# Optimization experiments

Measured on AMD Instinct MI355X. Metric: run time of the kernel, lower is better.

Reference implementation:

```python
import jax, jax.numpy as jnp
import numpy as np

# Module config (from init_kwargs): Occ3D-nuScenes volume
VOL_MIN = np.array([-40.0, -40.0, -1.0], dtype=np.float32)
VOXEL_SIZE = 0.4
GRID_SHAPE = (200, 200, 16)  # (vol_max - vol_min) / voxel_size
K = 6          # fixed per-gaussian window; covers radii <= 0.6m (bbox span <= 5 voxels)
N_GAUSS = 32768
N_DIMS = 16


def setup_inputs() -> dict:
    key = jax.random.key(0)
    k1, k2, k3, k4, k5 = jax.random.split(key, 5)
    # Means strictly inside the volume with 1m margin so bboxes stay in-grid.
    lo = jnp.array([-39.0, -39.0, 0.0], dtype=jnp.float32)
    hi = jnp.array([39.0, 39.0, 4.4], dtype=jnp.float32)
    means3d = jax.random.uniform(k1, (N_GAUSS, 3), minval=lo, maxval=hi, dtype=jnp.float32)
    # SPD covariances: Q diag(s) Q^T with eigenvalues in [0.01, 0.04]
    A = jax.random.normal(k2, (N_GAUSS, 3, 3), dtype=jnp.float32)
    Q, _ = jnp.linalg.qr(A)
    s = jax.random.uniform(k3, (N_GAUSS, 3), minval=0.01, maxval=0.04, dtype=jnp.float32)
    covs = jnp.einsum('nij,nj,nkj->nik', Q, s, Q)
    opacities = jax.random.uniform(k4, (N_GAUSS,), dtype=jnp.float32)
    features = jax.random.normal(k5, (N_GAUSS, N_DIMS), dtype=jnp.float32)
    return {"means3d": means3d, "covs": covs, "opacities": opacities, "features": features}


def reference(means3d, covs, opacities, features):
    N, D = features.shape
    dim_x, dim_y, dim_z = GRID_SHAPE
    total = dim_x * dim_y * dim_z
    vol_min = jnp.asarray(VOL_MIN)

    inv_covs = jnp.linalg.inv(covs)                                  # [N,3,3]
    radii = 3.0 * jnp.sqrt(jnp.diagonal(covs, axis1=-2, axis2=-1))   # [N,3]

    # Bounding box in voxel indices (trunc toward zero, like the triton .to(int32))
    s = (means3d - radii - vol_min) / VOXEL_SIZE
    e = (means3d + radii - vol_min) / VOXEL_SIZE
    start = jnp.maximum(0, s.astype(jnp.int32))                      # [N,3]
    end = jnp.minimum(jnp.array(GRID_SHAPE, jnp.int32), e.astype(jnp.int32) + 1)

    offs = jnp.arange(K, dtype=jnp.int32)
    ix = start[:, 0:1] + offs   # [N,K]
    iy = start[:, 1:2] + offs
    iz = start[:, 2:3] + offs
    mask = ((ix < end[:, 0:1])[:, :, None, None]
            & (iy < end[:, 1:2])[:, None, :, None]
            & (iz < end[:, 2:3])[:, None, None, :])                  # [N,K,K,K]

    # Voxel-corner minus mean offsets (matches kernel: x*vs + vol_min - m)
    px = ix.astype(means3d.dtype) * VOXEL_SIZE + vol_min[0] - means3d[:, 0:1]  # [N,K]
    py = iy.astype(means3d.dtype) * VOXEL_SIZE + vol_min[1] - means3d[:, 1:2]
    pz = iz.astype(means3d.dtype) * VOXEL_SIZE + vol_min[2] - means3d[:, 2:3]
    d = jnp.stack(jnp.broadcast_arrays(px[:, :, None, None],
                                       py[:, None, :, None],
                                       pz[:, None, None, :]), axis=-1)  # [N,K,K,K,3]

    mahal = jnp.einsum('nxyzi,nij,nxyzj->nxyz', d, inv_covs, d)      # [N,K,K,K]
    density = opacities[:, None, None, None] * jnp.exp(-0.5 * mahal)
    density = jnp.where(mask, density, 0.0)

    flat_idx = (ix[:, :, None, None] * (dim_y * dim_z)
                + iy[:, None, :, None] * dim_z
                + iz[:, None, None, :])                               # [N,K,K,K]
    idx = flat_idx.reshape(-1)

    grid_density = jnp.zeros((total,), density.dtype).at[idx].add(density.reshape(-1))

    contrib = density[..., None] * features[:, None, None, None, :]   # [N,K,K,K,D]
    grid_feats = jnp.zeros((total, D), density.dtype).at[:, -1].set(1e-5)
    grid_feats = grid_feats.at[idx].add(contrib.reshape(-1, D))
    grid_feats = grid_feats / jnp.clip(grid_density, 1e-6, None)[:, None]

    return grid_density.reshape(GRID_SHAPE), grid_feats.reshape(*GRID_SHAPE, D)
```

## Files before the change

kernel.cpp:

```cpp
#include <hip/hip_runtime.h>
#include <math.h>

constexpr int   GX = 200, GY = 200, GZ = 16;
constexpr int   TOTAL = GX * GY * GZ;
constexpr int   ND = 16;
constexpr int   KW = 6;
constexpr float VS = 0.4f;
constexpr float VMINX = -40.0f, VMINY = -40.0f, VMINZ = -1.0f;

constexpr int   TS = 4;
constexpr int   TX = 50, TY = 50;
constexpr int   NP = TX * TY;
constexpr int   REC = 32;
constexpr int   CAP = 128;
constexpr int   BR  = 8;
constexpr float NHL2E = -0.72134752044448170f;


__global__ __launch_bounds__(256) void gv_prep(
    const float* __restrict__ means, const float* __restrict__ covs,
    const float* __restrict__ opac,  const float* __restrict__ feats,
    float* __restrict__ gdata, int* __restrict__ counts,
    int* __restrict__ entries, int n)
{
    int g = blockIdx.x * 256 + threadIdx.x;
    if (g >= n) return;
    const float* cv = covs + (size_t)g * 9;
    float a = cv[0], b = cv[1], c = cv[2], d = cv[4], e = cv[5], f = cv[8];
    float A = d * f - e * e;
    float B = c * e - b * f;
    float C = b * e - c * d;
    float invdet = 1.0f / (a * A + b * B + c * C);
    float mx = means[g * 3 + 0], my = means[g * 3 + 1], mz = means[g * 3 + 2];
    float rx = 3.0f * sqrtf(a), ry = 3.0f * sqrtf(d), rz = 3.0f * sqrtf(f);
    int sx = max(0, (int)((mx - rx - VMINX) / VS));
    int sy = max(0, (int)((my - ry - VMINY) / VS));
    int sz = max(0, (int)((mz - rz - VMINZ) / VS));
    int ex = min(GX, (int)((mx + rx - VMINX) / VS) + 1); ex = min(ex, sx + KW);
    int ey = min(GY, (int)((my + ry - VMINY) / VS) + 1); ey = min(ey, sy + KW);
    int ez = min(GZ, (int)((mz + rz - VMINZ) / VS) + 1); ez = min(ez, sz + KW);

    float rec[REC];
    rec[0] = mx; rec[1] = my; rec[2] = mz; rec[3] = opac[g];
    rec[4] = (A * invdet) * NHL2E;
    rec[5] = (B * invdet) * (2.0f * NHL2E);
    rec[6] = (C * invdet) * (2.0f * NHL2E);
    rec[7] = ((a * f - c * c) * invdet) * NHL2E;
    rec[8] = ((b * c - a * e) * invdet) * (2.0f * NHL2E);
    rec[9] = ((a * d - b * b) * invdet) * NHL2E;
    rec[10] = __int_as_float(sx | (sy << 8) | (sz << 16));
    rec[11] = __int_as_float(ex | (ey << 8) | (ez << 16));
    rec[12] = 0.0f; rec[13] = 0.0f; rec[14] = 0.0f; rec[15] = 0.0f;
    const float4* f4 = (const float4*)(feats + (size_t)g * ND);
#pragma unroll
    for (int q = 0; q < 4; ++q) {
        float4 v = f4[q];
        rec[16 + q * 4 + 0] = v.x; rec[16 + q * 4 + 1] = v.y;
        rec[16 + q * 4 + 2] = v.z; rec[16 + q * 4 + 3] = v.w;
    }
    float4* dst = (float4*)(gdata + (size_t)g * REC);
#pragma unroll
    for (int q = 0; q < 8; ++q) dst[q] = ((const float4*)rec)[q];

    int tx0 = sx >> 2, tx1 = (ex - 1) >> 2;
    int ty0 = sy >> 2, ty1 = (ey - 1) >> 2;
    for (int tx = tx0; tx <= tx1; ++tx)
        for (int ty = ty0; ty <= ty1; ++ty) {
            int tile = tx * TY + ty;
            int slot = atomicAdd(&counts[tile], 1);
            if (slot < CAP) entries[(size_t)tile * CAP + slot] = g;
        }
}

__global__ __launch_bounds__(256) void gv_tile(
    const float* __restrict__ gdata, const int* __restrict__ counts,
    const int* __restrict__ entries, float* __restrict__ out)
{
    const int wv   = threadIdx.x >> 6;
    const int lane = threadIdx.x & 63;
    const int p    = blockIdx.x * 4 + wv;
    const int pty  = p % TY;
    const int ptx  = p / TY;

    __shared__ float sbuf[4][2][BR * REC];

    const int lz2 = lane & 3, ly = (lane >> 2) & 3, lx = lane >> 4;
    const int ix = ptx * TS + lx, iy = pty * TS + ly;
    const float pxc = (float)ix * VS + VMINX;
    const float pyc = (float)iy * VS + VMINY;
    float pzcv[4];
    int   izv[4];
#pragma unroll
    for (int v = 0; v < 4; ++v) {
        izv[v] = v * 4 + lz2;
        pzcv[v] = (float)izv[v] * VS + VMINZ;
    }

    float accd[4];
    float accf[4][ND];
#pragma unroll
    for (int v = 0; v < 4; ++v) {
        accd[v] = 0.0f;
#pragma unroll
        for (int c = 0; c < ND; ++c) accf[v][c] = 0.0f;
        accf[v][ND - 1] = 1e-5f;
    }

    const int cnt = __builtin_amdgcn_readfirstlane(min(counts[p], CAP));
    const int* __restrict__ el = entries + (size_t)p * CAP;

    const int rlane = lane >> 3;
    const int flane = lane & 7;
    const int wslot = rlane * REC + flane * 4;

    if (cnt > 0) {
        const int nb = (cnt + BR - 1) >> 3;
        float* b0 = &sbuf[wv][0][0];
        float* b1 = &sbuf[wv][1][0];

        int id0 = el[min(rlane, cnt - 1)];
        float4 v0 = *(const float4*)(gdata + (size_t)id0 * REC + flane * 4);
        *(float4*)(b0 + wslot) = v0;
        int idn = el[min(BR + rlane, cnt - 1)];
        float4 vn = *(const float4*)(gdata + (size_t)idn * REC + flane * 4);
        int idn2 = el[min(2 * BR + rlane, cnt - 1)];

        for (int b = 0; b < nb; ++b) {
            if (b + 1 < nb) {
                float* dst = ((b + 1) & 1) ? b1 : b0;
                *(float4*)(dst + wslot) = vn;
                vn = *(const float4*)(gdata + (size_t)idn2 * REC + flane * 4);
                idn2 = el[min((b + 3) * BR + rlane, cnt - 1)];
            }
            const float* rb = (b & 1) ? b1 : b0;
            const int rn = min(BR, cnt - b * BR);
            for (int r = 0; r < rn; ++r) {
                const float* rec = rb + r * REC;
                float4 q2 = *(const float4*)(rec + 8);
                int spk = __float_as_int(q2.z), epk = __float_as_int(q2.w);
                int sx = spk & 255, sy = (spk >> 8) & 255, sz = (spk >> 16) & 255;
                int ex = epk & 255, ey = (epk >> 8) & 255, ez = (epk >> 16) & 255;
                bool in_xy = (ix >= sx) & (ix < ex) & (iy >= sy) & (iy < ey);

                float4 m  = *(const float4*)(rec);
                float4 q0 = *(const float4*)(rec + 4);
                float px = pxc - m.x;
                float py = pyc - m.y;
                float a1 = fmaf(q0.y, py, q0.x * px);
                float A0 = fmaf(q0.w * py, py, a1 * px);
                float B0 = fmaf(q2.x, py, q0.z * px);

                float4 f0 = *(const float4*)(rec + 16);
                float4 f1 = *(const float4*)(rec + 20);
                float4 f2 = *(const float4*)(rec + 24);
                float4 f3 = *(const float4*)(rec + 28);

                const int qlo = sz >> 2, qhi = (ez - 1) >> 2;
#pragma unroll
                for (int v = 0; v < 4; ++v) {
                    if (v < qlo || v > qhi) continue;
                    float pz = pzcv[v] - m.z;
                    float q = fmaf(pz, fmaf(q2.y, pz, B0), A0);
                    float dens = m.w * __builtin_amdgcn_exp2f(q);
                    bool in = in_xy & (izv[v] >= sz) & (izv[v] < ez);
                    dens = in ? dens : 0.0f;
                    accd[v] += dens;
                    accf[v][0]  = fmaf(dens, f0.x, accf[v][0]);
                    accf[v][1]  = fmaf(dens, f0.y, accf[v][1]);
                    accf[v][2]  = fmaf(dens, f0.z, accf[v][2]);
                    accf[v][3]  = fmaf(dens, f0.w, accf[v][3]);
                    accf[v][4]  = fmaf(dens, f1.x, accf[v][4]);
                    accf[v][5]  = fmaf(dens, f1.y, accf[v][5]);
                    accf[v][6]  = fmaf(dens, f1.z, accf[v][6]);
                    accf[v][7]  = fmaf(dens, f1.w, accf[v][7]);
                    accf[v][8]  = fmaf(dens, f2.x, accf[v][8]);
                    accf[v][9]  = fmaf(dens, f2.y, accf[v][9]);
                    accf[v][10] = fmaf(dens, f2.z, accf[v][10]);
                    accf[v][11] = fmaf(dens, f2.w, accf[v][11]);
                    accf[v][12] = fmaf(dens, f3.x, accf[v][12]);
                    accf[v][13] = fmaf(dens, f3.y, accf[v][13]);
                    accf[v][14] = fmaf(dens, f3.z, accf[v][14]);
                    accf[v][15] = fmaf(dens, f3.w, accf[v][15]);
                }
            }
        }
    }

#pragma unroll
    for (int v = 0; v < 4; ++v) {
        const int flat = (ix * GY + iy) * GZ + izv[v];
        out[flat] = accd[v];
        float inv = 1.0f / fmaxf(accd[v], 1e-6f);
        float4* fo = (float4*)(out + TOTAL + (size_t)flat * ND);
#pragma unroll
        for (int q = 0; q < 4; ++q) {
            float4 w;
            w.x = accf[v][q * 4 + 0] * inv;
            w.y = accf[v][q * 4 + 1] * inv;
            w.z = accf[v][q * 4 + 2] * inv;
            w.w = accf[v][q * 4 + 3] * inv;
            fo[q] = w;
        }
    }
}

extern "C" void kernel_launch(void* const* d_in, const int* in_sizes, int n_in,
                              void* d_out, int out_size, void* d_ws, size_t ws_size,
                              hipStream_t stream) {
    const float* means = (const float*)d_in[0];
    const float* covs  = (const float*)d_in[1];
    const float* opac  = (const float*)d_in[2];
    const float* feats = (const float*)d_in[3];
    float* out = (float*)d_out;
    const int n = in_sizes[2];

    float* gdata   = (float*)d_ws;
    int*   counts  = (int*)(gdata + (size_t)n * REC);
    int*   entries = counts + ((NP + 63) & ~63);

    hipMemsetAsync(counts, 0, NP * sizeof(int), stream);
    gv_prep<<<(n + 255) / 256, 256, 0, stream>>>(means, covs, opac, feats,
                                                 gdata, counts, entries, n);
    gv_tile<<<NP / 4, 256, 0, stream>>>(gdata, counts, entries, out);
}
```

Measured before the change: 112.4 us.

## Fuse memset, prep and tile kernels into one cooperative persistent kernel

Replaces the memset plus two kernel launches with a single cooperative kernel of 512 blocks that zeroes counts, builds the per-gaussian records and tile lists, and uses grid-wide syncs between phases. The tile phase becomes persistent, with each wavefront pulling tiles from an atomic cursor for dynamic load balancing. This aims to remove launch and inter-kernel gaps. In exchange it adds two grid barriers, cursor atomics and a fixed grid size that may reduce occupancy for the prep phase.

```diff
diff --git a/kernel.cpp b/kernel.cpp
--- a/kernel.cpp
+++ b/kernel.cpp
@@ -1,5 +1,8 @@
 #include <hip/hip_runtime.h>
+#include <hip/hip_cooperative_groups.h>
 #include <math.h>
+
+namespace cg = cooperative_groups;
 
 constexpr int   GX = 200, GY = 200, GZ = 16;
 constexpr int   TOTAL = GX * GY * GZ;
@@ -14,80 +17,80 @@
 constexpr int   REC = 32;
 constexpr int   CAP = 128;
 constexpr int   BR  = 8;
+constexpr int   GRID = 512;
 constexpr float NHL2E = -0.72134752044448170f;
 
 
-__global__ __launch_bounds__(256) void gv_prep(
+__global__ __launch_bounds__(256) void gv_fused(
     const float* __restrict__ means, const float* __restrict__ covs,
     const float* __restrict__ opac,  const float* __restrict__ feats,
     float* __restrict__ gdata, int* __restrict__ counts,
-    int* __restrict__ entries, int n)
+    int* __restrict__ entries, int* __restrict__ cursor,
+    float* __restrict__ out, int n)
 {
-    int g = blockIdx.x * 256 + threadIdx.x;
-    if (g >= n) return;
-    const float* cv = covs + (size_t)g * 9;
-    float a = cv[0], b = cv[1], c = cv[2], d = cv[4], e = cv[5], f = cv[8];
-    float A = d * f - e * e;
-    float B = c * e - b * f;
-    float C = b * e - c * d;
-    float invdet = 1.0f / (a * A + b * B + c * C);
-    float mx = means[g * 3 + 0], my = means[g * 3 + 1], mz = means[g * 3 + 2];
-    float rx = 3.0f * sqrtf(a), ry = 3.0f * sqrtf(d), rz = 3.0f * sqrtf(f);
-    int sx = max(0, (int)((mx - rx - VMINX) / VS));
-    int sy = max(0, (int)((my - ry - VMINY) / VS));
-    int sz = max(0, (int)((mz - rz - VMINZ) / VS));
-    int ex = min(GX, (int)((mx + rx - VMINX) / VS) + 1); ex = min(ex, sx + KW);
-    int ey = min(GY, (int)((my + ry - VMINY) / VS) + 1); ey = min(ey, sy + KW);
-    int ez = min(GZ, (int)((mz + rz - VMINZ) / VS) + 1); ez = min(ez, sz + KW);
-
-    float rec[REC];
-    rec[0] = mx; rec[1] = my; rec[2] = mz; rec[3] = opac[g];
-    rec[4] = (A * invdet) * NHL2E;
-    rec[5] = (B * invdet) * (2.0f * NHL2E);
-    rec[6] = (C * invdet) * (2.0f * NHL2E);
-    rec[7] = ((a * f - c * c) * invdet) * NHL2E;
-    rec[8] = ((b * c - a * e) * invdet) * (2.0f * NHL2E);
-    rec[9] = ((a * d - b * b) * invdet) * NHL2E;
-    rec[10] = __int_as_float(sx | (sy << 8) | (sz << 16));
-    rec[11] = __int_as_float(ex | (ey << 8) | (ez << 16));
-    rec[12] = 0.0f; rec[13] = 0.0f; rec[14] = 0.0f; rec[15] = 0.0f;
-    const float4* f4 = (const float4*)(feats + (size_t)g * ND);
-#pragma unroll
-    for (int q = 0; q < 4; ++q) {
-        float4 v = f4[q];
-        rec[16 + q * 4 + 0] = v.x; rec[16 + q * 4 + 1] = v.y;
-        rec[16 + q * 4 + 2] = v.z; rec[16 + q * 4 + 3] = v.w;
+    cg::grid_group grid = cg::this_grid();
+    const int tid = blockIdx.x * 256 + threadIdx.x;
+    const int nth = GRID * 256;
+
+    for (int i = tid; i < NP; i += nth) counts[i] = 0;
+    if (tid == 0) *cursor = 0;
+    grid.sync();
+
+    for (int g = tid; g < n; g += nth) {
+        const float* cv = covs + (size_t)g * 9;
+        float a = cv[0], b = cv[1], c = cv[2], d = cv[4], e = cv[5], f = cv[8];
+        float A = d * f - e * e;
+        float B = c * e - b * f;
+        float C = b * e - c * d;
+        float invdet = 1.0f / (a * A + b * B + c * C);
+        float mx = means[g * 3 + 0], my = means[g * 3 + 1], mz = means[g * 3 + 2];
+        float rx = 3.0f * sqrtf(a), ry = 3.0f * sqrtf(d), rz = 3.0f * sqrtf(f);
+        int sx = max(0, (int)((mx - rx - VMINX) / VS));
+        int sy = max(0, (int)((my - ry - VMINY) / VS));
+        int sz = max(0, (int)((mz - rz - VMINZ) / VS));
+        int ex = min(GX, (int)((mx + rx - VMINX) / VS) + 1); ex = min(ex, sx + KW);
+        int ey = min(GY, (int)((my + ry - VMINY) / VS) + 1); ey = min(ey, sy + KW);
+        int ez = min(GZ, (int)((mz + rz - VMINZ) / VS) + 1); ez = min(ez, sz + KW);
+
+        float rec[REC];
+        rec[0] = mx; rec[1] = my; rec[2] = mz; rec[3] = opac[g];
+        rec[4] = (A * invdet) * NHL2E;
+        rec[5] = (B * invdet) * (2.0f * NHL2E);
+        rec[6] = (C * invdet) * (2.0f * NHL2E);
+        rec[7] = ((a * f - c * c) * invdet) * NHL2E;
+        rec[8] = ((b * c - a * e) * invdet) * (2.0f * NHL2E);
+        rec[9] = ((a * d - b * b) * invdet) * NHL2E;
+        rec[10] = __int_as_float(sx | (sy << 8) | (sz << 16));
+        rec[11] = __int_as_float(ex | (ey << 8) | (ez << 16));
+        rec[12] = 0.0f; rec[13] = 0.0f; rec[14] = 0.0f; rec[15] = 0.0f;
+        const float4* f4 = (const float4*)(feats + (size_t)g * ND);
+#pragma unroll
+        for (int q = 0; q < 4; ++q) {
+            float4 v = f4[q];
+            rec[16 + q * 4 + 0] = v.x; rec[16 + q * 4 + 1] = v.y;
+            rec[16 + q * 4 + 2] = v.z; rec[16 + q * 4 + 3] = v.w;
+        }
+        float4* dst = (float4*)(gdata + (size_t)g * REC);
+#pragma unroll
+        for (int q = 0; q < 8; ++q) dst[q] = ((const float4*)rec)[q];
+
+        int tx0 = sx >> 2, tx1 = (ex - 1) >> 2;
+        int ty0 = sy >> 2, ty1 = (ey - 1) >> 2;
+        for (int tx = tx0; tx <= tx1; ++tx)
+            for (int ty = ty0; ty <= ty1; ++ty) {
+                int tile = tx * TY + ty;
+                int slot = atomicAdd(&counts[tile], 1);
+                if (slot < CAP) entries[(size_t)tile * CAP + slot] = g;
+            }
     }
-    float4* dst = (float4*)(gdata + (size_t)g * REC);
-#pragma unroll
-    for (int q = 0; q < 8; ++q) dst[q] = ((const float4*)rec)[q];
-
-    int tx0 = sx >> 2, tx1 = (ex - 1) >> 2;
-    int ty0 = sy >> 2, ty1 = (ey - 1) >> 2;
-    for (int tx = tx0; tx <= tx1; ++tx)
-        for (int ty = ty0; ty <= ty1; ++ty) {
-            int tile = tx * TY + ty;
-            int slot = atomicAdd(&counts[tile], 1);
-            if (slot < CAP) entries[(size_t)tile * CAP + slot] = g;
-        }
-}
-
-__global__ __launch_bounds__(256) void gv_tile(
-    const float* __restrict__ gdata, const int* __restrict__ counts,
-    const int* __restrict__ entries, float* __restrict__ out)
-{
+    grid.sync();
+
     const int wv   = threadIdx.x >> 6;
     const int lane = threadIdx.x & 63;
-    const int p    = blockIdx.x * 4 + wv;
-    const int pty  = p % TY;
-    const int ptx  = p / TY;
 
     __shared__ float sbuf[4][2][BR * REC];
 
     const int lz2 = lane & 3, ly = (lane >> 2) & 3, lx = lane >> 4;
-    const int ix = ptx * TS + lx, iy = pty * TS + ly;
-    const float pxc = (float)ix * VS + VMINX;
-    const float pyc = (float)iy * VS + VMINY;
     float pzcv[4];
     int   izv[4];
 #pragma unroll
@@ -95,111 +98,122 @@
         izv[v] = v * 4 + lz2;
         pzcv[v] = (float)izv[v] * VS + VMINZ;
     }
-
-    float accd[4];
-    float accf[4][ND];
-#pragma unroll
-    for (int v = 0; v < 4; ++v) {
-        accd[v] = 0.0f;
-#pragma unroll
-        for (int c = 0; c < ND; ++c) accf[v][c] = 0.0f;
-        accf[v][ND - 1] = 1e-5f;
-    }
-
-    const int cnt = __builtin_amdgcn_readfirstlane(min(counts[p], CAP));
-    const int* __restrict__ el = entries + (size_t)p * CAP;
-
     const int rlane = lane >> 3;
     const int flane = lane & 7;
     const int wslot = rlane * REC + flane * 4;
 
-    if (cnt > 0) {
-        const int nb = (cnt + BR - 1) >> 3;
-        float* b0 = &sbuf[wv][0][0];
-        float* b1 = &sbuf[wv][1][0];
-
-        int id0 = el[min(rlane, cnt - 1)];
-        float4 v0 = *(const float4*)(gdata + (size_t)id0 * REC + flane * 4);
-        *(float4*)(b0 + wslot) = v0;
-        int idn = el[min(BR + rlane, cnt - 1)];
-        float4 vn = *(const float4*)(gdata + (size_t)idn * REC + flane * 4);
-        int idn2 = el[min(2 * BR + rlane, cnt - 1)];
-
-        for (int b = 0; b < nb; ++b) {
-            if (b + 1 < nb) {
-                float* dst = ((b + 1) & 1) ? b1 : b0;
-                *(float4*)(dst + wslot) = vn;
-                vn = *(const float4*)(gdata + (size_t)idn2 * REC + flane * 4);
-                idn2 = el[min((b + 3) * BR + rlane, cnt - 1)];
-            }
-            const float* rb = (b & 1) ? b1 : b0;
-            const int rn = min(BR, cnt - b * BR);
-            for (int r = 0; r < rn; ++r) {
-                const float* rec = rb + r * REC;
-                float4 q2 = *(const float4*)(rec + 8);
-                int spk = __float_as_int(q2.z), epk = __float_as_int(q2.w);
-                int sx = spk & 255, sy = (spk >> 8) & 255, sz = (spk >> 16) & 255;
-                int ex = epk & 255, ey = (epk >> 8) & 255, ez = (epk >> 16) & 255;
-                bool in_xy = (ix >= sx) & (ix < ex) & (iy >= sy) & (iy < ey);
-
-                float4 m  = *(const float4*)(rec);
-                float4 q0 = *(const float4*)(rec + 4);
-                float px = pxc - m.x;
-                float py = pyc - m.y;
-                float a1 = fmaf(q0.y, py, q0.x * px);
-                float A0 = fmaf(q0.w * py, py, a1 * px);
-                float B0 = fmaf(q2.x, py, q0.z * px);
-
-                float4 f0 = *(const float4*)(rec + 16);
-                float4 f1 = *(const float4*)(rec + 20);
-                float4 f2 = *(const float4*)(rec + 24);
-                float4 f3 = *(const float4*)(rec + 28);
-
-                const int qlo = sz >> 2, qhi = (ez - 1) >> 2;
-#pragma unroll
-                for (int v = 0; v < 4; ++v) {
-                    if (v < qlo || v > qhi) continue;
-                    float pz = pzcv[v] - m.z;
-                    float q = fmaf(pz, fmaf(q2.y, pz, B0), A0);
-                    float dens = m.w * __builtin_amdgcn_exp2f(q);
-                    bool in = in_xy & (izv[v] >= sz) & (izv[v] < ez);
-                    dens = in ? dens : 0.0f;
-                    accd[v] += dens;
-                    accf[v][0]  = fmaf(dens, f0.x, accf[v][0]);
-                    accf[v][1]  = fmaf(dens, f0.y, accf[v][1]);
-                    accf[v][2]  = fmaf(dens, f0.z, accf[v][2]);
-                    accf[v][3]  = fmaf(dens, f0.w, accf[v][3]);
-                    accf[v][4]  = fmaf(dens, f1.x, accf[v][4]);
-                    accf[v][5]  = fmaf(dens, f1.y, accf[v][5]);
-                    accf[v][6]  = fmaf(dens, f1.z, accf[v][6]);
-                    accf[v][7]  = fmaf(dens, f1.w, accf[v][7]);
-                    accf[v][8]  = fmaf(dens, f2.x, accf[v][8]);
-                    accf[v][9]  = fmaf(dens, f2.y, accf[v][9]);
-                    accf[v][10] = fmaf(dens, f2.z, accf[v][10]);
-                    accf[v][11] = fmaf(dens, f2.w, accf[v][11]);
-                    accf[v][12] = fmaf(dens, f3.x, accf[v][12]);
-                    accf[v][13] = fmaf(dens, f3.y, accf[v][13]);
-                    accf[v][14] = fmaf(dens, f3.z, accf[v][14]);
-                    accf[v][15] = fmaf(dens, f3.w, accf[v][15]);
+    while (true) {
+        int p = 0;
+        if (lane == 0) p = atomicAdd(cursor, 1);
+        p = __shfl(p, 0, 64);
+        if (p >= NP) break;
+        const int pty = p % TY;
+        const int ptx = p / TY;
+        const int ix = ptx * TS + lx, iy = pty * TS + ly;
+        const float pxc = (float)ix * VS + VMINX;
+        const float pyc = (float)iy * VS + VMINY;
+
+        float accd[4];
+        float accf[4][ND];
+#pragma unroll
+        for (int v = 0; v < 4; ++v) {
+            accd[v] = 0.0f;
+#pragma unroll
+            for (int c = 0; c < ND; ++c) accf[v][c] = 0.0f;
+            accf[v][ND - 1] = 1e-5f;
+        }
+
+        const int cnt = __builtin_amdgcn_readfirstlane(min(counts[p], CAP));
+        const int* __restrict__ el = entries + (size_t)p * CAP;
+
+        if (cnt > 0) {
+            const int nb = (cnt + BR - 1) >> 3;
+            float* b0 = &sbuf[wv][0][0];
+            float* b1 = &sbuf[wv][1][0];
+
+            int id0 = el[min(rlane, cnt - 1)];
+            float4 v0 = *(const float4*)(gdata + (size_t)id0 * REC + flane * 4);
+            *(float4*)(b0 + wslot) = v0;
+            int idn = el[min(BR + rlane, cnt - 1)];
+            float4 vn = *(const float4*)(gdata + (size_t)idn * REC + flane * 4);
+            int idn2 = el[min(2 * BR + rlane, cnt - 1)];
+
+            for (int b = 0; b < nb; ++b) {
+                if (b + 1 < nb) {
+                    float* dstb = ((b + 1) & 1) ? b1 : b0;
+                    *(float4*)(dstb + wslot) = vn;
+                    vn = *(const float4*)(gdata + (size_t)idn2 * REC + flane * 4);
+                    idn2 = el[min((b + 3) * BR + rlane, cnt - 1)];
+                }
+                const float* rb = (b & 1) ? b1 : b0;
+                const int rn = min(BR, cnt - b * BR);
+                for (int r = 0; r < rn; ++r) {
+                    const float* rec = rb + r * REC;
+                    float4 q2 = *(const float4*)(rec + 8);
+                    int spk = __float_as_int(q2.z), epk = __float_as_int(q2.w);
+                    int sx = spk & 255, sy = (spk >> 8) & 255, sz = (spk >> 16) & 255;
+                    int ex = epk & 255, ey = (epk >> 8) & 255, ez = (epk >> 16) & 255;
+                    bool in_xy = (ix >= sx) & (ix < ex) & (iy >= sy) & (iy < ey);
+
+                    float4 m  = *(const float4*)(rec);
+                    float4 q0 = *(const float4*)(rec + 4);
+                    float px = pxc - m.x;
+                    float py = pyc - m.y;
+                    float a1 = fmaf(q0.y, py, q0.x * px);
+                    float A0 = fmaf(q0.w * py, py, a1 * px);
+                    float B0 = fmaf(q2.x, py, q0.z * px);
+
+                    float4 f0 = *(const float4*)(rec + 16);
+                    float4 f1 = *(const float4*)(rec + 20);
+                    float4 f2 = *(const float4*)(rec + 24);
+                    float4 f3 = *(const float4*)(rec + 28);
+
+                    const int qlo = sz >> 2, qhi = (ez - 1) >> 2;
+#pragma unroll
+                    for (int v = 0; v < 4; ++v) {
+                        if (v < qlo || v > qhi) continue;
+                        float pz = pzcv[v] - m.z;
+                        float q = fmaf(pz, fmaf(q2.y, pz, B0), A0);
+                        float dens = m.w * __builtin_amdgcn_exp2f(q);
+                        bool in = in_xy & (izv[v] >= sz) & (izv[v] < ez);
+                        dens = in ? dens : 0.0f;
+                        accd[v] += dens;
+                        accf[v][0]  = fmaf(dens, f0.x, accf[v][0]);
+                        accf[v][1]  = fmaf(dens, f0.y, accf[v][1]);
+                        accf[v][2]  = fmaf(dens, f0.z, accf[v][2]);
+                        accf[v][3]  = fmaf(dens, f0.w, accf[v][3]);
+                        accf[v][4]  = fmaf(dens, f1.x, accf[v][4]);
+                        accf[v][5]  = fmaf(dens, f1.y, accf[v][5]);
+                        accf[v][6]  = fmaf(dens, f1.z, accf[v][6]);
+                        accf[v][7]  = fmaf(dens, f1.w, accf[v][7]);
+                        accf[v][8]  = fmaf(dens, f2.x, accf[v][8]);
+                        accf[v][9]  = fmaf(dens, f2.y, accf[v][9]);
+                        accf[v][10] = fmaf(dens, f2.z, accf[v][10]);
+                        accf[v][11] = fmaf(dens, f2.w, accf[v][11]);
+                        accf[v][12] = fmaf(dens, f3.x, accf[v][12]);
+                        accf[v][13] = fmaf(dens, f3.y, accf[v][13]);
+                        accf[v][14] = fmaf(dens, f3.z, accf[v][14]);
+                        accf[v][15] = fmaf(dens, f3.w, accf[v][15]);
+                    }
                 }
             }
         }
-    }
-
-#pragma unroll
-    for (int v = 0; v < 4; ++v) {
-        const int flat = (ix * GY + iy) * GZ + izv[v];
-        out[flat] = accd[v];
-        float inv = 1.0f / fmaxf(accd[v], 1e-6f);
-        float4* fo = (float4*)(out + TOTAL + (size_t)flat * ND);
-#pragma unroll
-        for (int q = 0; q < 4; ++q) {
-            float4 w;
-            w.x = accf[v][q * 4 + 0] * inv;
-            w.y = accf[v][q * 4 + 1] * inv;
-            w.z = accf[v][q * 4 + 2] * inv;
-            w.w = accf[v][q * 4 + 3] * inv;
-            fo[q] = w;
+
+#pragma unroll
+        for (int v = 0; v < 4; ++v) {
+            const int flat = (ix * GY + iy) * GZ + izv[v];
+            out[flat] = accd[v];
+            float inv = 1.0f / fmaxf(accd[v], 1e-6f);
+            float4* fo = (float4*)(out + TOTAL + (size_t)flat * ND);
+#pragma unroll
+            for (int q = 0; q < 4; ++q) {
+                float4 w;
+                w.x = accf[v][q * 4 + 0] * inv;
+                w.y = accf[v][q * 4 + 1] * inv;
+                w.z = accf[v][q * 4 + 2] * inv;
+                w.w = accf[v][q * 4 + 3] * inv;
+                fo[q] = w;
+            }
         }
     }
 }
@@ -212,14 +226,16 @@
     const float* opac  = (const float*)d_in[2];
     const float* feats = (const float*)d_in[3];
     float* out = (float*)d_out;
-    const int n = in_sizes[2];
+    int n = in_sizes[2];
 
     float* gdata   = (float*)d_ws;
     int*   counts  = (int*)(gdata + (size_t)n * REC);
     int*   entries = counts + ((NP + 63) & ~63);
-
-    hipMemsetAsync(counts, 0, NP * sizeof(int), stream);
-    gv_prep<<<(n + 255) / 256, 256, 0, stream>>>(means, covs, opac, feats,
-                                                 gdata, counts, entries, n);
-    gv_tile<<<NP / 4, 256, 0, stream>>>(gdata, counts, entries, out);
+    int*   cursor  = entries + (size_t)NP * CAP;
+
+    void* args[] = {(void*)&means, (void*)&covs, (void*)&opac, (void*)&feats,
+                    (void*)&gdata, (void*)&counts, (void*)&entries, (void*)&cursor,
+                    (void*)&out, (void*)&n};
+    hipLaunchCooperativeKernel((const void*)gv_fused, dim3(GRID), dim3(256),
+                               args, 0, stream);
 }
```

After: 242.7 us. 116% more time.
